# Performance work log

Hardware: AMD Instinct MI355X
Metric: run time of the kernel (lower is better)

The kernel has to match this reference:

```python
import math
import jax, jax.numpy as jnp
import numpy as np

B = 16; ENC_S = 64; ENC_T = 96
SCALE = 64; POOL = 16; DM = 256; NH = 16
E_LAYERS = 3; D_LAYERS = 2; DFF = 1024
OUT_S = 64; OUT_T = 32
LN_EPS = 1e-5


def _pe(d_model, length):
    pos = np.arange(length, dtype=np.float32)[:, None]
    div = np.exp(np.arange(0, d_model, 2, dtype=np.float32) * (-math.log(10000.0) / d_model))
    pe = np.zeros((length, d_model), np.float32)
    pe[:, 0::2] = np.sin(pos * div)
    pe[:, 1::2] = np.cos(pos * div)
    return jnp.asarray(pe)


def _conv1d_circ(x, w, b):
    # x: (N, C, L), w: (O, C, 3); torch Conv1d(padding=1, padding_mode='circular')
    xp = jnp.pad(x, ((0, 0), (0, 0), (1, 1)), mode='wrap')
    y = jax.lax.conv_general_dilated(xp, w, (1,), 'VALID',
                                     dimension_numbers=('NCH', 'OIH', 'NCH'))
    return y + b[None, :, None]


def _layernorm(x, w, b):
    mu = jnp.mean(x, -1, keepdims=True)
    var = jnp.var(x, -1, keepdims=True)
    return (x - mu) * jax.lax.rsqrt(var + LN_EPS) * w + b


def _data_embedding(x, sproj_w, sproj_b, scproj_w, scproj_b, tok_w, tok_b):
    Bb = x.shape[0]
    h = _conv1d_circ(jnp.swapaxes(x, 1, 2), sproj_w, sproj_b)       # (B, enc_t, enc_t)
    h = _conv1d_circ(h, scproj_w, scproj_b)                          # (B, scale, enc_t)
    h = _conv1d_circ(jnp.swapaxes(h, 1, 2), scproj_w, scproj_b)     # (B, scale, scale)
    h = h.reshape(Bb * SCALE, 1, SCALE)
    tok = jnp.swapaxes(_conv1d_circ(h, tok_w, tok_b), 1, 2)          # (B*scale, scale, dm)
    emb = tok + _pe(DM, SCALE)[None]
    return emb.reshape(Bb, SCALE, SCALE, DM)


def _lin_attn(q, k, v, causal):
    # q,k,v: (Bp, L, H, E); k/v adaptively avg-pooled over L to POOL (L % POOL == 0)
    Bp, L, H, E = q.shape
    win = L // POOL
    kp = k.reshape(Bp, POOL, win, H, E).mean(axis=2)
    vp = v.reshape(Bp, POOL, win, H, E).mean(axis=2)
    scores = jnp.einsum('blhe,bshe->bhls', q, kp)      # (Bp, H, L, POOL)
    if causal:
        m = jnp.arange(POOL)[None, :] > jnp.arange(L)[:, None]
        scores = jnp.where(m[None, None], -jnp.inf, scores)
    A = jax.nn.softmax(scores / math.sqrt(E), axis=-1)
    return jnp.einsum('bhls,bshd->blhd', A, vp)


def _st_attn(x, kv, Wq, bq, Wo, bo, causal):
    Bb, T, S, dm = x.shape
    H = NH // 2
    proj = lambda z: z @ Wq.T + bq
    # faithful to source: query_projection used for q, k AND v; views are flat reshapes
    qt = proj(x.reshape(Bb * S, T, dm)).reshape(Bb * S, T, H, -1)
    qs = proj(x.reshape(Bb * T, S, dm)).reshape(Bb * T, S, H, -1)
    kt = proj(kv.reshape(Bb * S, T, dm)).reshape(Bb * S, T, H, -1)
    ks = proj(kv.reshape(Bb * T, S, dm)).reshape(Bb * T, S, H, -1)
    out_t = _lin_attn(qt, kt, kt, causal).reshape(Bb, S, T, -1)
    out_s = _lin_attn(qs, ks, ks, causal).reshape(Bb, S, T, -1)
    out = jnp.concatenate([out_t, out_s], axis=-1).reshape(Bb, S * T, 2 * dm)
    out = out @ Wo.T + bo
    return out.reshape(Bb, T, S, dm)


def _ffn(x, c1w, c1b, c2w, c2b):
    # conv1d kernel_size=1 over the T axis of (B*S, T, dm) == pointwise GEMM
    Bb, T, S, dm = x.shape
    y = x.reshape(Bb * S, T, dm)
    y = jax.nn.gelu(jnp.einsum('ntd,fd->ntf', y, c1w) + c1b, approximate=False)
    y = jnp.einsum('ntf,df->ntd', y, c2w) + c2b
    return y.reshape(Bb, T, S, dm)


def _forward(x_enc, x_dec,
             enc_sproj_w, enc_sproj_b, enc_scproj_w, enc_scproj_b, enc_tok_w, enc_tok_b,
             dec_sproj_w, dec_sproj_b, dec_scproj_w, dec_scproj_b, dec_tok_w, dec_tok_b,
             e_Wq, e_bq, e_Wo, e_bo, e_c1w, e_c1b, e_c2w, e_c2b,
             e_ln1w, e_ln1b, e_ln2w, e_ln2b, enc_norm_w, enc_norm_b,
             d_sWq, d_sbq, d_sWo, d_sbo, d_cWq, d_cbq, d_cWo, d_cbo,
             d_c1w, d_c1b, d_c2w, d_c2b,
             d_ln1w, d_ln1b, d_ln2w, d_ln2b, d_ln3w, d_ln3b,
             dec_norm_w, dec_norm_b, proj_w, proj_b):
    enc = _data_embedding(x_enc, enc_sproj_w, enc_sproj_b, enc_scproj_w, enc_scproj_b, enc_tok_w, enc_tok_b)
    for i in range(E_LAYERS):
        h = enc + _st_attn(enc, enc, e_Wq[i], e_bq[i], e_Wo[i], e_bo[i], False)
        h = _layernorm(h, e_ln1w[i], e_ln1b[i])
        enc = _layernorm(h + _ffn(h, e_c1w[i], e_c1b[i], e_c2w[i], e_c2b[i]), e_ln2w[i], e_ln2b[i])
    enc = _layernorm(enc, enc_norm_w, enc_norm_b)
    dec = _data_embedding(x_dec, dec_sproj_w, dec_sproj_b, dec_scproj_w, dec_scproj_b, dec_tok_w, dec_tok_b)
    for i in range(D_LAYERS):
        h = dec + _st_attn(dec, dec, d_sWq[i], d_sbq[i], d_sWo[i], d_sbo[i], True)
        h = _layernorm(h, d_ln1w[i], d_ln1b[i])
        h = h + _st_attn(h, enc, d_cWq[i], d_cbq[i], d_cWo[i], d_cbo[i], False)
        h = _layernorm(h, d_ln2w[i], d_ln2b[i])
        dec = _layernorm(h + _ffn(h, d_c1w[i], d_c1b[i], d_c2w[i], d_c2b[i]), d_ln3w[i], d_ln3b[i])
    dec = _layernorm(dec, dec_norm_w, dec_norm_b)
    dec = dec.mean(axis=2)                 # (B, scale, dm)
    out = dec @ proj_w.T + proj_b          # (B, scale, out_s)
    return out[:, -OUT_T:, :]


def setup_inputs() -> dict:
    keys = iter(jax.random.split(jax.random.key(0), 80))
    def nrm(shape, s=0.02):
        return jax.random.normal(next(keys), shape, jnp.float32) * s
    E, D = E_LAYERS, D_LAYERS
    inp = {
        'x_enc': nrm((B, ENC_T, ENC_S), 1.0),
        'x_dec': nrm((B, ENC_T, ENC_S), 1.0),
    }
    for p in ('enc', 'dec'):
        inp[p + '_sproj_w'] = nrm((ENC_T, ENC_S, 3)); inp[p + '_sproj_b'] = nrm((ENC_T,))
        inp[p + '_scproj_w'] = nrm((SCALE, ENC_T, 3)); inp[p + '_scproj_b'] = nrm((SCALE,))
        inp[p + '_tok_w'] = nrm((DM, 1, 3), 0.1); inp[p + '_tok_b'] = nrm((DM,))
    inp.update(
        e_Wq=nrm((E, DM, DM)), e_bq=nrm((E, DM)),
        e_Wo=nrm((E, DM, 2 * DM)), e_bo=nrm((E, DM)),
        e_c1w=nrm((E, DFF, DM)), e_c1b=nrm((E, DFF)),
        e_c2w=nrm((E, DM, DFF)), e_c2b=nrm((E, DM)),
        e_ln1w=jnp.ones((E, DM)), e_ln1b=jnp.zeros((E, DM)),
        e_ln2w=jnp.ones((E, DM)), e_ln2b=jnp.zeros((E, DM)),
        enc_norm_w=jnp.ones((DM,)), enc_norm_b=jnp.zeros((DM,)),
        d_sWq=nrm((D, DM, DM)), d_sbq=nrm((D, DM)),
        d_sWo=nrm((D, DM, 2 * DM)), d_sbo=nrm((D, DM)),
        d_cWq=nrm((D, DM, DM)), d_cbq=nrm((D, DM)),
        d_cWo=nrm((D, DM, 2 * DM)), d_cbo=nrm((D, DM)),
        d_c1w=nrm((D, DFF, DM)), d_c1b=nrm((D, DFF)),
        d_c2w=nrm((D, DM, DFF)), d_c2b=nrm((D, DM)),
        d_ln1w=jnp.ones((D, DM)), d_ln1b=jnp.zeros((D, DM)),
        d_ln2w=jnp.ones((D, DM)), d_ln2b=jnp.zeros((D, DM)),
        d_ln3w=jnp.ones((D, DM)), d_ln3b=jnp.zeros((D, DM)),
        dec_norm_w=jnp.ones((DM,)), dec_norm_b=jnp.zeros((DM,)),
        proj_w=nrm((OUT_S, DM)), proj_b=nrm((OUT_S,)),
    )
    return inp


def reference(x_enc, x_dec,
              enc_sproj_w, enc_sproj_b, enc_scproj_w, enc_scproj_b, enc_tok_w, enc_tok_b,
              dec_sproj_w, dec_sproj_b, dec_scproj_w, dec_scproj_b, dec_tok_w, dec_tok_b,
              e_Wq, e_bq, e_Wo, e_bo, e_c1w, e_c1b, e_c2w, e_c2b,
              e_ln1w, e_ln1b, e_ln2w, e_ln2b, enc_norm_w, enc_norm_b,
              d_sWq, d_sbq, d_sWo, d_sbo, d_cWq, d_cbq, d_cWo, d_cbo,
              d_c1w, d_c1b, d_c2w, d_c2b,
              d_ln1w, d_ln1b, d_ln2w, d_ln2b, d_ln3w, d_ln3b,
              dec_norm_w, dec_norm_b, proj_w, proj_b):
    return _forward(x_enc, x_dec,
                    enc_sproj_w, enc_sproj_b, enc_scproj_w, enc_scproj_b, enc_tok_w, enc_tok_b,
                    dec_sproj_w, dec_sproj_b, dec_scproj_w, dec_scproj_b, dec_tok_w, dec_tok_b,
                    e_Wq, e_bq, e_Wo, e_bo, e_c1w, e_c1b, e_c2w, e_c2b,
                    e_ln1w, e_ln1b, e_ln2w, e_ln2b, enc_norm_w, enc_norm_b,
                    d_sWq, d_sbq, d_sWo, d_sbo, d_cWq, d_cbq, d_cWo, d_cbo,
                    d_c1w, d_c1b, d_c2w, d_c2b,
                    d_ln1w, d_ln1b, d_ln2w, d_ln2b, d_ln3w, d_ln3b,
                    dec_norm_w, dec_norm_b, proj_w, proj_b)
```

## Files before the change

### kernel.cpp

```cpp
#include <hip/hip_runtime.h>


typedef unsigned short u16;
typedef short s16;
typedef __attribute__((ext_vector_type(8))) s16 bfrag;
typedef __attribute__((ext_vector_type(4))) float f32x4;

__device__ __forceinline__ float b2f(u16 u) {
  union { float f; unsigned int i; } v; v.i = ((unsigned int)u) << 16; return v.f;
}
__device__ __forceinline__ u16 f2b(float f) {
  union { float f; unsigned int i; } v; v.f = f;
  unsigned int x = v.i;
  return (u16)((x + 0x7FFFu + ((x >> 16) & 1u)) >> 16);
}

__device__ __forceinline__ void gload16(const void* g, void* l) {
  __builtin_amdgcn_global_load_lds(
      (const __attribute__((address_space(1))) unsigned int*)g,
      (__attribute__((address_space(3))) unsigned int*)l, 16, 0, 0);
}

__global__ void ws_signal(float* out, float v) { out[0] = v; }

__global__ void cvt_bf(const float* __restrict__ src, u16* __restrict__ dst, int n) {
  int i = blockIdx.x * 256 + threadIdx.x;
  if (i < n) dst[i] = f2b(src[i]);
}
__global__ void weff_bf(const float* __restrict__ Wo, u16* __restrict__ W) {
  int n = blockIdx.x, k = threadIdx.x;
  W[n * 256 + k] = f2b(Wo[n * 512 + k] + Wo[n * 512 + 256 + k]);
}

__global__ void pe_kernel(float* __restrict__ pe) {
  int l = blockIdx.x, d = threadIdx.x;
  int i = d >> 1;
  float div = expf((float)(2 * i) * (-9.210340371976184f / 256.0f));
  float ang = (float)l * div;
  pe[l * 256 + d] = (d & 1) ? cosf(ang) : sinf(ang);
}

__global__ void conv_sproj(const float* __restrict__ x, const float* __restrict__ w,
                           const float* __restrict__ bias, float* __restrict__ h1) {
  int o = blockIdx.x, b = blockIdx.y, l = threadIdx.x;
  const float* wo = w + o * 192;
  const float* xb = x + (size_t)b * 96 * 64;
  float acc = bias[o];
#pragma unroll
  for (int k = 0; k < 3; ++k) {
    int lp = l + k - 1; if (lp < 0) lp += 96; if (lp >= 96) lp -= 96;
    const float* xr = xb + lp * 64;
    for (int c = 0; c < 64; ++c) acc = fmaf(xr[c], wo[c * 3 + k], acc);
  }
  h1[((size_t)b * 96 + o) * 96 + l] = acc;
}

__global__ void conv_scproj_t(const float* __restrict__ h1, const float* __restrict__ w,
                              const float* __restrict__ bias, float* __restrict__ h2) {
  int o = blockIdx.x, b = blockIdx.y, l = threadIdx.x;
  const float* wo = w + o * 288;
  const float* hb = h1 + (size_t)b * 96 * 96;
  float acc = bias[o];
#pragma unroll
  for (int k = 0; k < 3; ++k) {
    int lp = l + k - 1; if (lp < 0) lp += 96; if (lp >= 96) lp -= 96;
    for (int c = 0; c < 96; ++c) acc = fmaf(hb[c * 96 + lp], wo[c * 3 + k], acc);
  }
  h2[((size_t)b * 64 + o) * 96 + l] = acc;
}

__global__ void conv_scproj_s(const float* __restrict__ h2, const float* __restrict__ w,
                              const float* __restrict__ bias, float* __restrict__ h3) {
  int o = blockIdx.x, b = blockIdx.y, l = threadIdx.x;
  const float* wo = w + o * 288;
  const float* hb = h2 + (size_t)b * 64 * 96;
  float acc = bias[o];
#pragma unroll
  for (int k = 0; k < 3; ++k) {
    int lp = l + k - 1; if (lp < 0) lp += 64; if (lp >= 64) lp -= 64;
    for (int c = 0; c < 96; ++c) acc = fmaf(hb[lp * 96 + c], wo[c * 3 + k], acc);
  }
  h3[((size_t)b * 64 + o) * 64 + l] = acc;
}

__global__ void tok_embed(const float* __restrict__ h3, const float* __restrict__ w,
                          const float* __restrict__ bias, const float* __restrict__ pe,
                          u16* __restrict__ E) {
  int g = blockIdx.x, d = threadIdx.x;
  __shared__ float row[64];
  if (d < 64) row[d] = h3[(size_t)g * 64 + d];
  __syncthreads();
  float w0 = w[d * 3], w1 = w[d * 3 + 1], w2 = w[d * 3 + 2], bd = bias[d];
  for (int j = 0; j < 64; ++j) {
    int jm = (j + 63) & 63, jp = (j + 1) & 63;
    float v = bd + row[jm] * w0 + row[j] * w1 + row[jp] * w2 + pe[j * 256 + d];
    E[((size_t)g * 64 + j) * 256 + d] = f2b(v);
  }
}

template <int ACT>
__global__ __launch_bounds__(256) void mfma_gemm(const u16* __restrict__ A,
                                                 const u16* __restrict__ W,
                                                 const float* __restrict__ bias,
                                                 u16* __restrict__ C, int N, int K) {
  __shared__ s16 As[4096];
  __shared__ s16 Bs[4096];
  int t = threadIdx.x;
  int wave = t >> 6, lane = t & 63;
  int wr = wave >> 1, wc = wave & 1;
  int row0 = blockIdx.y * 128, col0 = blockIdx.x * 128;
  int kc = (lane >> 4) & 3, rr = lane & 15;
  const u16* Ap0 = A + (size_t)(row0 + wave * 16 + rr) * K + kc * 8;
  const u16* Ap1 = A + (size_t)(row0 + (wave + 4) * 16 + rr) * K + kc * 8;
  const u16* Bp0 = W + (size_t)(col0 + wave * 16 + rr) * K + kc * 8;
  const u16* Bp1 = W + (size_t)(col0 + (wave + 4) * 16 + rr) * K + kc * 8;
  s16* lA0 = As + wave * 512;
  s16* lA1 = As + (wave + 4) * 512;
  s16* lB0 = Bs + wave * 512;
  s16* lB1 = Bs + (wave + 4) * 512;
  f32x4 acc[4][4];
#pragma unroll
  for (int m = 0; m < 4; ++m)
#pragma unroll
    for (int n = 0; n < 4; ++n) acc[m][n] = (f32x4){0.f, 0.f, 0.f, 0.f};
  for (int k0 = 0; k0 < K; k0 += 32) {
    gload16(Ap0 + k0, lA0);
    gload16(Ap1 + k0, lA1);
    gload16(Bp0 + k0, lB0);
    gload16(Bp1 + k0, lB1);
    __syncthreads();
    bfrag af[4], bf[4];
#pragma unroll
    for (int m = 0; m < 4; ++m) af[m] = *(const bfrag*)(As + ((wr * 4 + m) * 64 + lane) * 8);
#pragma unroll
    for (int n = 0; n < 4; ++n) bf[n] = *(const bfrag*)(Bs + ((wc * 4 + n) * 64 + lane) * 8);
#pragma unroll
    for (int m = 0; m < 4; ++m)
#pragma unroll
      for (int n = 0; n < 4; ++n)
        acc[m][n] = __builtin_amdgcn_mfma_f32_16x16x32_bf16(af[m], bf[n], acc[m][n], 0, 0, 0);
    __syncthreads();
  }
  int rbase = row0 + wr * 64 + ((lane >> 4) << 2);
  int cbase = col0 + wc * 64 + (lane & 15);
#pragma unroll
  for (int n = 0; n < 4; ++n) {
    int col = cbase + n * 16;
    float bcol = bias[col];
#pragma unroll
    for (int m = 0; m < 4; ++m) {
#pragma unroll
      for (int r = 0; r < 4; ++r) {
        float v = acc[m][n][r] + bcol;
        if (ACT == 1) v = 0.5f * v * (1.0f + erff(v * 0.7071067811865476f));
        C[(size_t)(rbase + m * 16 + r) * N + col] = f2b(v);
      }
    }
  }
}

__global__ __launch_bounds__(512) void mfma_gemm_resln(const u16* __restrict__ X,
                                                       const u16* __restrict__ W,
                                                       const float* __restrict__ bias,
                                                       u16* __restrict__ R,
                                                       const float* __restrict__ lnw,
                                                       const float* __restrict__ lnb,
                                                       int K) {
  __shared__ s16 As[4096];
  __shared__ s16 Bs[8192];
  __shared__ float pls[128][4][2];
  int t = threadIdx.x;
  int wave = t >> 6, lane = t & 63;
  int wr = wave >> 2, wc = wave & 3;
  int row0 = blockIdx.x * 128;
  int kc = (lane >> 4) & 3, rr = lane & 15;
  const u16* Xp = X + (size_t)(row0 + wave * 16 + rr) * K + kc * 8;
  const u16* Wp0 = W + (size_t)(wave * 16 + rr) * K + kc * 8;
  const u16* Wp1 = W + (size_t)((wave + 8) * 16 + rr) * K + kc * 8;
  s16* lA = As + wave * 512;
  s16* lB0 = Bs + wave * 512;
  s16* lB1 = Bs + (wave + 8) * 512;
  f32x4 acc[4][4];
#pragma unroll
  for (int m = 0; m < 4; ++m)
#pragma unroll
    for (int n = 0; n < 4; ++n) acc[m][n] = (f32x4){0.f, 0.f, 0.f, 0.f};
  for (int k0 = 0; k0 < K; k0 += 32) {
    gload16(Xp + k0, lA);
    gload16(Wp0 + k0, lB0);
    gload16(Wp1 + k0, lB1);
    __syncthreads();
    bfrag af[4], bf[4];
#pragma unroll
    for (int m = 0; m < 4; ++m) af[m] = *(const bfrag*)(As + ((wr * 4 + m) * 64 + lane) * 8);
#pragma unroll
    for (int n = 0; n < 4; ++n) bf[n] = *(const bfrag*)(Bs + ((wc * 4 + n) * 64 + lane) * 8);
#pragma unroll
    for (int m = 0; m < 4; ++m)
#pragma unroll
      for (int n = 0; n < 4; ++n)
        acc[m][n] = __builtin_amdgcn_mfma_f32_16x16x32_bf16(af[m], bf[n], acc[m][n], 0, 0, 0);
    __syncthreads();
  }
  int g4 = (lane >> 4) << 2;
  int cl = lane & 15;
  float lw[4], lb[4], bc[4];
#pragma unroll
  for (int n = 0; n < 4; ++n) {
    int col = wc * 64 + n * 16 + cl;
    bc[n] = bias[col]; lw[n] = lnw[col]; lb[n] = lnb[col];
  }
#pragma unroll
  for (int m = 0; m < 4; ++m) {
#pragma unroll
    for (int r = 0; r < 4; ++r) {
      int row = row0 + wr * 64 + m * 16 + g4 + r;
      float s = 0.f, s2 = 0.f;
#pragma unroll
      for (int n = 0; n < 4; ++n) {
        int col = wc * 64 + n * 16 + cl;
        float v = acc[m][n][r] + bc[n] + b2f(R[(size_t)row * 256 + col]);
        acc[m][n][r] = v;
        s += v; s2 = fmaf(v, v, s2);
      }
#pragma unroll
      for (int o = 1; o < 16; o <<= 1) { s += __shfl_xor(s, o); s2 += __shfl_xor(s2, o); }
      if (cl == 0) {
        int rl = wr * 64 + m * 16 + g4 + r;
        pls[rl][wc][0] = s; pls[rl][wc][1] = s2;
      }
    }
  }
  __syncthreads();
#pragma unroll
  for (int m = 0; m < 4; ++m) {
#pragma unroll
    for (int r = 0; r < 4; ++r) {
      int rl = wr * 64 + m * 16 + g4 + r;
      float s = pls[rl][0][0] + pls[rl][1][0] + pls[rl][2][0] + pls[rl][3][0];
      float s2 = pls[rl][0][1] + pls[rl][1][1] + pls[rl][2][1] + pls[rl][3][1];
      float mu = s * (1.0f / 256.0f);
      float var = fmaxf(s2 * (1.0f / 256.0f) - mu * mu, 0.0f);
      float rs = rsqrtf(var + 1e-5f);
      int row = row0 + wr * 64 + m * 16 + g4 + r;
#pragma unroll
      for (int n = 0; n < 4; ++n) {
        int col = wc * 64 + n * 16 + cl;
        R[(size_t)row * 256 + col] = f2b((acc[m][n][r] - mu) * rs * lw[n] + lb[n]);
      }
    }
  }
}

template <int CROSS, int CAUSAL>
__global__ __launch_bounds__(512) void lin_attn(u16* __restrict__ Q,
                                                const u16* __restrict__ KP) {
  __shared__ u16 qs[64 * 264];
  __shared__ float kpool[16][260];
  int p = blockIdx.x, t = threadIdx.x;
  u16* Qg = Q + (size_t)p * 16384;
#pragma unroll
  for (int i = 0; i < 4; ++i) {
    int idx = i * 512 + t;
    int row = idx >> 5, slot = idx & 31;
    *(uint4*)(qs + row * 264 + slot * 8) = *(const uint4*)(Qg + row * 256 + slot * 8);
  }
  __syncthreads();
  if (CROSS) {
    for (int idx = t; idx < 4096; idx += 512) {
      int s = idx >> 8, d = idx & 255;
      kpool[s][d] = b2f(KP[((size_t)p * 16 + s) * 256 + d]);
    }
  } else {
    for (int idx = t; idx < 4096; idx += 512) {
      int s = idx >> 8, d = idx & 255;
      const u16* b0 = qs + (4 * s) * 264 + d;
      kpool[s][d] = 0.25f * (b2f(b0[0]) + b2f(b0[264]) + b2f(b0[528]) + b2f(b0[792]));
    }
  }
  __syncthreads();
  int h = t >> 6, l = t & 63;
  u16* q = qs + l * 264 + h * 32;
  float qr[32];
#pragma unroll
  for (int e = 0; e < 32; e += 4) {
    ushort4 v = *(const ushort4*)&q[e];
    qr[e] = b2f(v.x); qr[e + 1] = b2f(v.y); qr[e + 2] = b2f(v.z); qr[e + 3] = b2f(v.w);
  }
  float sc[16], mx = -INFINITY;
#pragma unroll
  for (int s = 0; s < 16; ++s) {
    const float* kp = &kpool[s][h * 32];
    float d = 0.f;
#pragma unroll
    for (int e = 0; e < 32; ++e) d = fmaf(qr[e], kp[e], d);
    d *= 0.17677669529663687f;
    if (CAUSAL && s > l) d = -INFINITY;
    sc[s] = d; mx = fmaxf(mx, d);
  }
  float sum = 0.f;
#pragma unroll
  for (int s = 0; s < 16; ++s) { sc[s] = expf(sc[s] - mx); sum += sc[s]; }
  float inv = 1.0f / sum;
  float o[32] = {};
#pragma unroll
  for (int s = 0; s < 16; ++s) {
    float a = sc[s] * inv;
    const float* vp = &kpool[s][h * 32];
#pragma unroll
    for (int e = 0; e < 32; ++e) o[e] = fmaf(a, vp[e], o[e]);
  }
#pragma unroll
  for (int e = 0; e < 32; e += 4) {
    ushort4 v;
    v.x = f2b(o[e]); v.y = f2b(o[e + 1]); v.z = f2b(o[e + 2]); v.w = f2b(o[e + 3]);
    *(ushort4*)&q[e] = v;
  }
  __syncthreads();
#pragma unroll
  for (int i = 0; i < 4; ++i) {
    int idx = i * 512 + t;
    int row = idx >> 5, slot = idx & 31;
    *(uint4*)(Qg + row * 256 + slot * 8) = *(const uint4*)(qs + row * 264 + slot * 8);
  }
}

__global__ __launch_bounds__(256) void ln_bf(u16* __restrict__ X,
                                             const float* __restrict__ w,
                                             const float* __restrict__ b) {
  int lane = threadIdx.x & 63, wv = threadIdx.x >> 6;
  size_t row = (size_t)blockIdx.x * 4 + wv;
  size_t off = row * 256 + lane * 4;
  ushort4 xv = *(const ushort4*)(X + off);
  float v0 = b2f(xv.x), v1 = b2f(xv.y), v2 = b2f(xv.z), v3 = b2f(xv.w);
  float s = v0 + v1 + v2 + v3;
  float s2 = v0 * v0 + v1 * v1 + v2 * v2 + v3 * v3;
#pragma unroll
  for (int o = 32; o; o >>= 1) { s += __shfl_xor(s, o); s2 += __shfl_xor(s2, o); }
  float mu = s * (1.0f / 256.0f);
  float var = fmaxf(s2 * (1.0f / 256.0f) - mu * mu, 0.0f);
  float rs = rsqrtf(var + 1e-5f);
  float4 w4 = *(const float4*)(w + lane * 4);
  float4 b4 = *(const float4*)(b + lane * 4);
  ushort4 o4;
  o4.x = f2b((v0 - mu) * rs * w4.x + b4.x);
  o4.y = f2b((v1 - mu) * rs * w4.y + b4.y);
  o4.z = f2b((v2 - mu) * rs * w4.z + b4.z);
  o4.w = f2b((v3 - mu) * rs * w4.w + b4.w);
  *(ushort4*)(X + off) = o4;
}

__global__ void pool_bf(const u16* __restrict__ A, u16* __restrict__ P) {
  int r = blockIdx.x, d = threadIdx.x;
  int g = r >> 4, s = r & 15;
  const u16* src = A + ((size_t)g * 64 + 4 * (size_t)s) * 256 + d;
  float v = 0.25f * (b2f(src[0]) + b2f(src[256]) + b2f(src[512]) + b2f(src[768]));
  P[(size_t)r * 256 + d] = f2b(v);
}

__global__ __launch_bounds__(256) void mean_proj_bf(const u16* __restrict__ X,
                                                    const float* __restrict__ pw,
                                                    const float* __restrict__ pb,
                                                    float* __restrict__ out) {
  int bid = blockIdx.x;
  int b = bid >> 5, ii = bid & 31;
  int i = 32 + ii;
  __shared__ float md[256];
  int d = threadIdx.x;
  const u16* base = X + ((size_t)b * 64 + i) * 64 * 256 + d;
  float s = 0.f;
  for (int j = 0; j < 64; ++j) s += b2f(base[(size_t)j * 256]);
  md[d] = s * (1.0f / 64.0f);
  __syncthreads();
  if (d < 64) {
    float acc = pb[d];
    const float* wr = pw + d * 256;
    for (int k = 0; k < 256; ++k) acc = fmaf(md[k], wr[k], acc);
    out[((size_t)b * 32 + ii) * 64 + d] = acc;
  }
}

extern "C" void kernel_launch(void* const* d_in, const int* in_sizes, int n_in,
                              void* d_out, int out_size, void* d_ws, size_t ws_size,
                              hipStream_t stream) {
  (void)in_sizes; (void)out_size;
  if (n_in < 50) return;

  const float* x_enc = (const float*)d_in[0];
  const float* x_dec = (const float*)d_in[1];
  const float* enc_sproj_w = (const float*)d_in[2];
  const float* enc_sproj_b = (const float*)d_in[3];
  const float* enc_scproj_w = (const float*)d_in[4];
  const float* enc_scproj_b = (const float*)d_in[5];
  const float* enc_tok_w = (const float*)d_in[6];
  const float* enc_tok_b = (const float*)d_in[7];
  const float* dec_sproj_w = (const float*)d_in[8];
  const float* dec_sproj_b = (const float*)d_in[9];
  const float* dec_scproj_w = (const float*)d_in[10];
  const float* dec_scproj_b = (const float*)d_in[11];
  const float* dec_tok_w = (const float*)d_in[12];
  const float* dec_tok_b = (const float*)d_in[13];
  const float* e_Wq = (const float*)d_in[14];
  const float* e_bq = (const float*)d_in[15];
  const float* e_Wo = (const float*)d_in[16];
  const float* e_bo = (const float*)d_in[17];
  const float* e_c1w = (const float*)d_in[18];
  const float* e_c1b = (const float*)d_in[19];
  const float* e_c2w = (const float*)d_in[20];
  const float* e_c2b = (const float*)d_in[21];
  const float* e_ln1w = (const float*)d_in[22];
  const float* e_ln1b = (const float*)d_in[23];
  const float* e_ln2w = (const float*)d_in[24];
  const float* e_ln2b = (const float*)d_in[25];
  const float* enc_norm_w = (const float*)d_in[26];
  const float* enc_norm_b = (const float*)d_in[27];
  const float* d_sWq = (const float*)d_in[28];
  const float* d_sbq = (const float*)d_in[29];
  const float* d_sWo = (const float*)d_in[30];
  const float* d_sbo = (const float*)d_in[31];
  const float* d_cWq = (const float*)d_in[32];
  const float* d_cbq = (const float*)d_in[33];
  const float* d_cWo = (const float*)d_in[34];
  const float* d_cbo = (const float*)d_in[35];
  const float* d_c1w = (const float*)d_in[36];
  const float* d_c1b = (const float*)d_in[37];
  const float* d_c2w = (const float*)d_in[38];
  const float* d_c2b = (const float*)d_in[39];
  const float* d_ln1w = (const float*)d_in[40];
  const float* d_ln1b = (const float*)d_in[41];
  const float* d_ln2w = (const float*)d_in[42];
  const float* d_ln2b = (const float*)d_in[43];
  const float* d_ln3w = (const float*)d_in[44];
  const float* d_ln3b = (const float*)d_in[45];
  const float* dec_norm_w = (const float*)d_in[46];
  const float* dec_norm_b = (const float*)d_in[47];
  const float* proj_w = (const float*)d_in[48];
  const float* proj_b = (const float*)d_in[49];

  const size_t ACT = 16777216;
  const size_t POOLE = 4194304;
  const size_t WBN = 3538944;
  size_t base_need = (3 * ACT + 2 * POOLE + WBN) * 2 +
                     (size_t)(16384 + 147456 + 98304 + 65536) * 4;
  if (ws_size < base_need) {
    ws_signal<<<1, 1, 0, stream>>>((float*)d_out, (float)(ws_size >> 20));
    return;
  }
  char* wsb = (char*)d_ws;
  u16* A_enc = (u16*)wsb;  wsb += ACT * 2;
  u16* A_dec = (u16*)wsb;  wsb += ACT * 2;
  u16* T1 = (u16*)wsb;     wsb += ACT * 2;
  u16* PA = (u16*)wsb;     wsb += POOLE * 2;
  u16* PK = (u16*)wsb;     wsb += POOLE * 2;
  u16* WB = (u16*)wsb;     wsb += WBN * 2;
  float* PE = (float*)wsb;  wsb += 16384 * 4;
  float* EH1 = (float*)wsb; wsb += 147456 * 4;
  float* EH2 = (float*)wsb; wsb += 98304 * 4;
  float* EH3 = (float*)wsb; wsb += 65536 * 4;

  int hf_rows = 16384;
  u16* HF = T1;
  if (ws_size >= base_need + (size_t)65536 * 1024 * 2) {
    hf_rows = 65536; HF = (u16*)wsb;
  } else if (ws_size >= base_need + (size_t)32768 * 1024 * 2) {
    hf_rows = 32768; HF = (u16*)wsb;
  }

  u16* eWq = WB;
  u16* eWeff = WB + 196608;
  u16* eC1 = WB + 393216;
  u16* eC2 = WB + 1179648;
  u16* dB = WB + 1966080;
  u16* dsWq = dB;
  u16* dsWeff = dB + 131072;
  u16* dcWq = dB + 262144;
  u16* dcWeff = dB + 393216;
  u16* dC1 = dB + 524288;
  u16* dC2 = dB + 1048576;

  cvt_bf<<<768, 256, 0, stream>>>(e_Wq, eWq, 196608);
  cvt_bf<<<3072, 256, 0, stream>>>(e_c1w, eC1, 786432);
  cvt_bf<<<3072, 256, 0, stream>>>(e_c2w, eC2, 786432);
  cvt_bf<<<512, 256, 0, stream>>>(d_sWq, dsWq, 131072);
  cvt_bf<<<512, 256, 0, stream>>>(d_cWq, dcWq, 131072);
  cvt_bf<<<2048, 256, 0, stream>>>(d_c1w, dC1, 524288);
  cvt_bf<<<2048, 256, 0, stream>>>(d_c2w, dC2, 524288);
  for (int i = 0; i < 3; ++i)
    weff_bf<<<256, 256, 0, stream>>>(e_Wo + (size_t)i * 131072, eWeff + (size_t)i * 65536);
  for (int i = 0; i < 2; ++i) {
    weff_bf<<<256, 256, 0, stream>>>(d_sWo + (size_t)i * 131072, dsWeff + (size_t)i * 65536);
    weff_bf<<<256, 256, 0, stream>>>(d_cWo + (size_t)i * 131072, dcWeff + (size_t)i * 65536);
  }

  pe_kernel<<<64, 256, 0, stream>>>(PE);

  conv_sproj<<<dim3(96, 16), 96, 0, stream>>>(x_enc, enc_sproj_w, enc_sproj_b, EH1);
  conv_scproj_t<<<dim3(64, 16), 96, 0, stream>>>(EH1, enc_scproj_w, enc_scproj_b, EH2);
  conv_scproj_s<<<dim3(64, 16), 64, 0, stream>>>(EH2, enc_scproj_w, enc_scproj_b, EH3);
  tok_embed<<<1024, 256, 0, stream>>>(EH3, enc_tok_w, enc_tok_b, PE, A_enc);

  for (int i = 0; i < 3; ++i) {
    mfma_gemm<0><<<dim3(2, 512), 256, 0, stream>>>(A_enc, eWq + (size_t)i * 65536,
                                                   e_bq + i * 256, T1, 256, 256);
    lin_attn<0, 0><<<1024, 512, 0, stream>>>(T1, nullptr);
    mfma_gemm_resln<<<512, 512, 0, stream>>>(T1, eWeff + (size_t)i * 65536, e_bo + i * 256,
                                             A_enc, e_ln1w + i * 256, e_ln1b + i * 256, 256);
    for (int m0 = 0; m0 < 65536; m0 += hf_rows) {
      u16* Xc = A_enc + (size_t)m0 * 256;
      mfma_gemm<1><<<dim3(8, hf_rows / 128), 256, 0, stream>>>(
          Xc, eC1 + (size_t)i * 262144, e_c1b + i * 1024, HF, 1024, 256);
      mfma_gemm_resln<<<hf_rows / 128, 512, 0, stream>>>(
          HF, eC2 + (size_t)i * 262144, e_c2b + i * 256, Xc,
          e_ln2w + i * 256, e_ln2b + i * 256, 1024);
    }
  }
  ln_bf<<<16384, 256, 0, stream>>>(A_enc, enc_norm_w, enc_norm_b);
  pool_bf<<<16384, 256, 0, stream>>>(A_enc, PA);

  conv_sproj<<<dim3(96, 16), 96, 0, stream>>>(x_dec, dec_sproj_w, dec_sproj_b, EH1);
  conv_scproj_t<<<dim3(64, 16), 96, 0, stream>>>(EH1, dec_scproj_w, dec_scproj_b, EH2);
  conv_scproj_s<<<dim3(64, 16), 64, 0, stream>>>(EH2, dec_scproj_w, dec_scproj_b, EH3);
  tok_embed<<<1024, 256, 0, stream>>>(EH3, dec_tok_w, dec_tok_b, PE, A_dec);

  for (int i = 0; i < 2; ++i) {
    mfma_gemm<0><<<dim3(2, 512), 256, 0, stream>>>(A_dec, dsWq + (size_t)i * 65536,
                                                   d_sbq + i * 256, T1, 256, 256);
    lin_attn<0, 1><<<1024, 512, 0, stream>>>(T1, nullptr);
    mfma_gemm_resln<<<512, 512, 0, stream>>>(T1, dsWeff + (size_t)i * 65536, d_sbo + i * 256,
                                             A_dec, d_ln1w + i * 256, d_ln1b + i * 256, 256);
    mfma_gemm<0><<<dim3(2, 512), 256, 0, stream>>>(A_dec, dcWq + (size_t)i * 65536,
                                                   d_cbq + i * 256, T1, 256, 256);
    mfma_gemm<0><<<dim3(2, 128), 256, 0, stream>>>(PA, dcWq + (size_t)i * 65536,
                                                   d_cbq + i * 256, PK, 256, 256);
    lin_attn<1, 0><<<1024, 512, 0, stream>>>(T1, PK);
    mfma_gemm_resln<<<512, 512, 0, stream>>>(T1, dcWeff + (size_t)i * 65536, d_cbo + i * 256,
                                             A_dec, d_ln2w + i * 256, d_ln2b + i * 256, 256);
    for (int m0 = 0; m0 < 65536; m0 += hf_rows) {
      u16* Xc = A_dec + (size_t)m0 * 256;
      mfma_gemm<1><<<dim3(8, hf_rows / 128), 256, 0, stream>>>(
          Xc, dC1 + (size_t)i * 262144, d_c1b + i * 1024, HF, 1024, 256);
      mfma_gemm_resln<<<hf_rows / 128, 512, 0, stream>>>(
          HF, dC2 + (size_t)i * 262144, d_c2b + i * 256, Xc,
          d_ln3w + i * 256, d_ln3b + i * 256, 1024);
    }
  }
  ln_bf<<<16384, 256, 0, stream>>>(A_dec, dec_norm_w, dec_norm_b);

  mean_proj_bf<<<512, 256, 0, stream>>>(A_dec, proj_w, proj_b, (float*)d_out);
}
```

Before: 1.822 ms.

## Stage GEMM epilogues through LDS, swizzle block order, use tanh GELU

The GEMM and residual-LayerNorm epilogues now write results into shared memory in 32-row slabs and store them to global memory as 16-byte coalesced vectors, instead of scattered 2-byte stores. The residual tile is read into LDS the same way before the add and normalisation. Blocks are launched on a 1D grid remapped so consecutive workgroups are spread across XCDs, and the erf GELU is replaced by a tanh approximation computed with __expf. The extra barriers per slab add synchronisation, and the GELU approximation changes numerics slightly.

New measurement: 1.874 ms. +2.8%, slower.

```diff
diff --git a/kernel.cpp b/kernel.cpp
--- a/kernel.cpp
+++ b/kernel.cpp
@@ -13,6 +13,11 @@
   union { float f; unsigned int i; } v; v.f = f;
   unsigned int x = v.i;
   return (u16)((x + 0x7FFFu + ((x >> 16) & 1u)) >> 16);
+}
+__device__ __forceinline__ float gelu_f(float v) {
+  float u = 0.7978845608f * v * (1.0f + 0.044715f * v * v);
+  float e = __expf(2.0f * u);
+  return v * (1.0f - 1.0f / (e + 1.0f));
 }
 
 __device__ __forceinline__ void gload16(const void* g, void* l) {
@@ -98,17 +103,24 @@
   }
 }
 
-template <int ACT>
+template <int ACT, int NBX>
 __global__ __launch_bounds__(256) void mfma_gemm(const u16* __restrict__ A,
                                                  const u16* __restrict__ W,
                                                  const float* __restrict__ bias,
-                                                 u16* __restrict__ C, int N, int K) {
-  __shared__ s16 As[4096];
-  __shared__ s16 Bs[4096];
+                                                 u16* __restrict__ C, int N, int K,
+                                                 int nby) {
+  __shared__ s16 smem[8192];
+  s16* As = smem;
+  s16* Bs = smem + 4096;
+  constexpr int LB = (NBX == 8) ? 3 : 1;
+  int f = blockIdx.x;
+  int q = (NBX * nby) >> 3;
+  int w = (f & 7) * q + (f >> 3);
+  int bx = w & (NBX - 1), by = w >> LB;
   int t = threadIdx.x;
   int wave = t >> 6, lane = t & 63;
   int wr = wave >> 1, wc = wave & 1;
-  int row0 = blockIdx.y * 128, col0 = blockIdx.x * 128;
+  int row0 = by * 128, col0 = bx * 128;
   int kc = (lane >> 4) & 3, rr = lane & 15;
   const u16* Ap0 = A + (size_t)(row0 + wave * 16 + rr) * K + kc * 8;
   const u16* Ap1 = A + (size_t)(row0 + (wave + 4) * 16 + rr) * K + kc * 8;
@@ -141,20 +153,37 @@
         acc[m][n] = __builtin_amdgcn_mfma_f32_16x16x32_bf16(af[m], bf[n], acc[m][n], 0, 0, 0);
     __syncthreads();
   }
-  int rbase = row0 + wr * 64 + ((lane >> 4) << 2);
-  int cbase = col0 + wc * 64 + (lane & 15);
-#pragma unroll
-  for (int n = 0; n < 4; ++n) {
-    int col = cbase + n * 16;
-    float bcol = bias[col];
-#pragma unroll
-    for (int m = 0; m < 4; ++m) {
-#pragma unroll
-      for (int r = 0; r < 4; ++r) {
-        float v = acc[m][n][r] + bcol;
-        if (ACT == 1) v = 0.5f * v * (1.0f + erff(v * 0.7071067811865476f));
-        C[(size_t)(rbase + m * 16 + r) * N + col] = f2b(v);
+  s16* Cs = smem;
+  int g4 = (lane >> 4) << 2;
+  int cl = lane & 15;
+  float bc[4];
+#pragma unroll
+  for (int n = 0; n < 4; ++n) bc[n] = bias[col0 + wc * 64 + n * 16 + cl];
+#pragma unroll
+  for (int P = 0; P < 4; ++P) {
+    __syncthreads();
+    if (wr == (P >> 1)) {
+#pragma unroll
+      for (int mm = 0; mm < 2; ++mm) {
+        int m = (P & 1) * 2 + mm;
+#pragma unroll
+        for (int n = 0; n < 4; ++n) {
+#pragma unroll
+          for (int r = 0; r < 4; ++r) {
+            float v = acc[m][n][r] + bc[n];
+            if (ACT == 1) v = gelu_f(v);
+            Cs[(mm * 16 + g4 + r) * 136 + wc * 64 + n * 16 + cl] = (s16)f2b(v);
+          }
+        }
       }
+    }
+    __syncthreads();
+#pragma unroll
+    for (int it = 0; it < 2; ++it) {
+      int idx = it * 256 + t;
+      int lr = idx >> 4, slot = idx & 15;
+      *(uint4*)(C + (size_t)(row0 + P * 32 + lr) * N + col0 + slot * 8) =
+          *(const uint4*)(Cs + lr * 136 + slot * 8);
     }
   }
 }
@@ -166,9 +195,10 @@
                                                        const float* __restrict__ lnw,
                                                        const float* __restrict__ lnb,
                                                        int K) {
-  __shared__ s16 As[4096];
-  __shared__ s16 Bs[8192];
-  __shared__ float pls[128][4][2];
+  __shared__ s16 smem[12288];
+  __shared__ float pls[32][4][2];
+  s16* As = smem;
+  s16* Bs = smem + 4096;
   int t = threadIdx.x;
   int wave = t >> 6, lane = t & 63;
   int wr = wave >> 2, wc = wave & 3;
@@ -202,6 +232,7 @@
         acc[m][n] = __builtin_amdgcn_mfma_f32_16x16x32_bf16(af[m], bf[n], acc[m][n], 0, 0, 0);
     __syncthreads();
   }
+  s16* Rs = smem;
   int g4 = (lane >> 4) << 2;
   int cl = lane & 15;
   float lw[4], lb[4], bc[4];
@@ -211,43 +242,66 @@
     bc[n] = bias[col]; lw[n] = lnw[col]; lb[n] = lnb[col];
   }
 #pragma unroll
-  for (int m = 0; m < 4; ++m) {
-#pragma unroll
-    for (int r = 0; r < 4; ++r) {
-      int row = row0 + wr * 64 + m * 16 + g4 + r;
-      float s = 0.f, s2 = 0.f;
-#pragma unroll
-      for (int n = 0; n < 4; ++n) {
-        int col = wc * 64 + n * 16 + cl;
-        float v = acc[m][n][r] + bc[n] + b2f(R[(size_t)row * 256 + col]);
-        acc[m][n][r] = v;
-        s += v; s2 = fmaf(v, v, s2);
+  for (int P = 0; P < 4; ++P) {
+    bool own = (wr == (P >> 1));
+    __syncthreads();
+#pragma unroll
+    for (int it = 0; it < 2; ++it) {
+      int idx = it * 512 + t;
+      int lr = idx >> 5, slot = idx & 31;
+      *(uint4*)(Rs + lr * 264 + slot * 8) =
+          *(const uint4*)(R + (size_t)(row0 + P * 32 + lr) * 256 + slot * 8);
+    }
+    __syncthreads();
+    if (own) {
+#pragma unroll
+      for (int mm = 0; mm < 2; ++mm) {
+        int m = (P & 1) * 2 + mm;
+#pragma unroll
+        for (int r = 0; r < 4; ++r) {
+          int lr = mm * 16 + g4 + r;
+          float s = 0.f, s2 = 0.f;
+#pragma unroll
+          for (int n = 0; n < 4; ++n) {
+            float v = acc[m][n][r] + bc[n] +
+                      b2f((u16)Rs[lr * 264 + wc * 64 + n * 16 + cl]);
+            acc[m][n][r] = v;
+            s += v; s2 = fmaf(v, v, s2);
+          }
+#pragma unroll
+          for (int o = 1; o < 16; o <<= 1) { s += __shfl_xor(s, o); s2 += __shfl_xor(s2, o); }
+          if (cl == 0) { pls[lr][wc][0] = s; pls[lr][wc][1] = s2; }
+        }
       }
-#pragma unroll
-      for (int o = 1; o < 16; o <<= 1) { s += __shfl_xor(s, o); s2 += __shfl_xor(s2, o); }
-      if (cl == 0) {
-        int rl = wr * 64 + m * 16 + g4 + r;
-        pls[rl][wc][0] = s; pls[rl][wc][1] = s2;
+    }
+    __syncthreads();
+    if (own) {
+#pragma unroll
+      for (int mm = 0; mm < 2; ++mm) {
+        int m = (P & 1) * 2 + mm;
+#pragma unroll
+        for (int r = 0; r < 4; ++r) {
+          int lr = mm * 16 + g4 + r;
+          float s = pls[lr][0][0] + pls[lr][1][0] + pls[lr][2][0] + pls[lr][3][0];
+          float s2 = pls[lr][0][1] + pls[lr][1][1] + pls[lr][2][1] + pls[lr][3][1];
+          float mu = s * (1.0f / 256.0f);
+          float var = fmaxf(s2 * (1.0f / 256.0f) - mu * mu, 0.0f);
+          float rs = rsqrtf(var + 1e-5f);
+#pragma unroll
+          for (int n = 0; n < 4; ++n) {
+            Rs[lr * 264 + wc * 64 + n * 16 + cl] =
+                (s16)f2b((acc[m][n][r] - mu) * rs * lw[n] + lb[n]);
+          }
+        }
       }
     }
-  }
-  __syncthreads();
-#pragma unroll
-  for (int m = 0; m < 4; ++m) {
-#pragma unroll
-    for (int r = 0; r < 4; ++r) {
-      int rl = wr * 64 + m * 16 + g4 + r;
-      float s = pls[rl][0][0] + pls[rl][1][0] + pls[rl][2][0] + pls[rl][3][0];
-      float s2 = pls[rl][0][1] + pls[rl][1][1] + pls[rl][2][1] + pls[rl][3][1];
-      float mu = s * (1.0f / 256.0f);
-      float var = fmaxf(s2 * (1.0f / 256.0f) - mu * mu, 0.0f);
-      float rs = rsqrtf(var + 1e-5f);
-      int row = row0 + wr * 64 + m * 16 + g4 + r;
-#pragma unroll
-      for (int n = 0; n < 4; ++n) {
-        int col = wc * 64 + n * 16 + cl;
-        R[(size_t)row * 256 + col] = f2b((acc[m][n][r] - mu) * rs * lw[n] + lb[n]);
-      }
+    __syncthreads();
+#pragma unroll
+    for (int it = 0; it < 2; ++it) {
+      int idx = it * 512 + t;
+      int lr = idx >> 5, slot = idx & 31;
+      *(uint4*)(R + (size_t)(row0 + P * 32 + lr) * 256 + slot * 8) =
+          *(const uint4*)(Rs + lr * 264 + slot * 8);
     }
   }
 }
@@ -500,16 +554,17 @@
   tok_embed<<<1024, 256, 0, stream>>>(EH3, enc_tok_w, enc_tok_b, PE, A_enc);
 
   for (int i = 0; i < 3; ++i) {
-    mfma_gemm<0><<<dim3(2, 512), 256, 0, stream>>>(A_enc, eWq + (size_t)i * 65536,
-                                                   e_bq + i * 256, T1, 256, 256);
+    mfma_gemm<0, 2><<<1024, 256, 0, stream>>>(A_enc, eWq + (size_t)i * 65536,
+                                              e_bq + i * 256, T1, 256, 256, 512);
     lin_attn<0, 0><<<1024, 512, 0, stream>>>(T1, nullptr);
     mfma_gemm_resln<<<512, 512, 0, stream>>>(T1, eWeff + (size_t)i * 65536, e_bo + i * 256,
                                              A_enc, e_ln1w + i * 256, e_ln1b + i * 256, 256);
     for (int m0 = 0; m0 < 65536; m0 += hf_rows) {
       u16* Xc = A_enc + (size_t)m0 * 256;
-      mfma_gemm<1><<<dim3(8, hf_rows / 128), 256, 0, stream>>>(
-          Xc, eC1 + (size_t)i * 262144, e_c1b + i * 1024, HF, 1024, 256);
-      mfma_gemm_resln<<<hf_rows / 128, 512, 0, stream>>>(
+      int nby = hf_rows / 128;
+      mfma_gemm<1, 8><<<8 * nby, 256, 0, stream>>>(
+          Xc, eC1 + (size_t)i * 262144, e_c1b + i * 1024, HF, 1024, 256, nby);
+      mfma_gemm_resln<<<nby, 512, 0, stream>>>(
           HF, eC2 + (size_t)i * 262144, e_c2b + i * 256, Xc,
           e_ln2w + i * 256, e_ln2b + i * 256, 1024);
     }
@@ -523,23 +578,24 @@
   tok_embed<<<1024, 256, 0, stream>>>(EH3, dec_tok_w, dec_tok_b, PE, A_dec);
 
   for (int i = 0; i < 2; ++i) {
-    mfma_gemm<0><<<dim3(2, 512), 256, 0, stream>>>(A_dec, dsWq + (size_t)i * 65536,
-                                                   d_sbq + i * 256, T1, 256, 256);
+    mfma_gemm<0, 2><<<1024, 256, 0, stream>>>(A_dec, dsWq + (size_t)i * 65536,
+                                              d_sbq + i * 256, T1, 256, 256, 512);
     lin_attn<0, 1><<<1024, 512, 0, stream>>>(T1, nullptr);
     mfma_gemm_resln<<<512, 512, 0, stream>>>(T1, dsWeff + (size_t)i * 65536, d_sbo + i * 256,
                                              A_dec, d_ln1w + i * 256, d_ln1b + i * 256, 256);
-    mfma_gemm<0><<<dim3(2, 512), 256, 0, stream>>>(A_dec, dcWq + (size_t)i * 65536,
-                                                   d_cbq + i * 256, T1, 256, 256);
-    mfma_gemm<0><<<dim3(2, 128), 256, 0, stream>>>(PA, dcWq + (size_t)i * 65536,
-                                                   d_cbq + i * 256, PK, 256, 256);
+    mfma_gemm<0, 2><<<1024, 256, 0, stream>>>(A_dec, dcWq + (size_t)i * 65536,
+                                              d_cbq + i * 256, T1, 256, 256, 512);
+    mfma_gemm<0, 2><<<256, 256, 0, stream>>>(PA, dcWq + (size_t)i * 65536,
+                                             d_cbq + i * 256, PK, 256, 256, 128);
     lin_attn<1, 0><<<1024, 512, 0, stream>>>(T1, PK);
     mfma_gemm_resln<<<512, 512, 0, stream>>>(T1, dcWeff + (size_t)i * 65536, d_cbo + i * 256,
                                              A_dec, d_ln2w + i * 256, d_ln2b + i * 256, 256);
     for (int m0 = 0; m0 < 65536; m0 += hf_rows) {
       u16* Xc = A_dec + (size_t)m0 * 256;
-      mfma_gemm<1><<<dim3(8, hf_rows / 128), 256, 0, stream>>>(
-          Xc, dC1 + (size_t)i * 262144, d_c1b + i * 1024, HF, 1024, 256);
-      mfma_gemm_resln<<<hf_rows / 128, 512, 0, stream>>>(
+      int nby = hf_rows / 128;
+      mfma_gemm<1, 8><<<8 * nby, 256, 0, stream>>>(
+          Xc, dC1 + (size_t)i * 262144, d_c1b + i * 1024, HF, 1024, 256, nby);
+      mfma_gemm_resln<<<nby, 512, 0, stream>>>(
           HF, dC2 + (size_t)i * 262144, d_c2b + i * 256, Xc,
           d_ln3w + i * 256, d_ln3b + i * 256, 1024);
     }
```
